# Performance work log

Hardware: AMD Instinct MI355X
Metric: run time of the kernel (lower is better)

Reference implementation:

```python
import jax, jax.numpy as jnp
import numpy as np
from jax import lax

B, CH_G, H, W = 4, 64, 240, 320
C_FEA = 8           # must equal NUM for the 'cos' branch broadcast to work (as in the original)
NUM = 8             # k_f*k_f - 1
K_G = 3
IDX_REF = NUM // 2  # 4
AFF_GAMMA = 0.5     # aff_scale_const = gamma * num = 4.0 (TGASS)


def setup_inputs() -> dict:
    key = jax.random.key(0)
    k1, k2, k3, k4, k5 = jax.random.split(key, 5)
    guidance = jax.random.normal(k1, (B, CH_G, H, W), jnp.float32)
    gt_depth_conf = jax.random.uniform(k2, (B, 1, H, W), jnp.float32)
    tgtimg_fea = jax.random.normal(k3, (B, C_FEA, H // 2, W // 2), jnp.float32)
    # torch zero-inits these; use small random weights so offsets are nontrivial
    conv_w = jax.random.normal(k4, (3 * NUM, CH_G, K_G, K_G), jnp.float32) * 0.05
    conv_b = jax.random.normal(k5, (3 * NUM,), jnp.float32) * 0.01
    aff_scale_const = jnp.full((1,), AFF_GAMMA * NUM, jnp.float32)
    return {"guidance": guidance, "gt_depth_conf": gt_depth_conf, "tgtimg_fea": tgtimg_fea,
            "conv_w": conv_w, "conv_b": conv_b, "aff_scale_const": aff_scale_const}


def _bilinear_zeros(img, x, y):
    """img: (C,Hh,Ww); x,y: (P,) absolute pixel coords. Bilinear, zero outside (== grid_sample
    align_corners=True padding_mode='zeros' and the deformable-conv im2col sampling)."""
    C, Hh, Ww = img.shape
    x0 = jnp.floor(x)
    y0 = jnp.floor(y)
    wx = x - x0
    wy = y - y0

    def g(xi, yi):
        valid = (xi >= 0) & (xi <= Ww - 1) & (yi >= 0) & (yi <= Hh - 1)
        xc = jnp.clip(xi, 0, Ww - 1).astype(jnp.int32)
        yc = jnp.clip(yi, 0, Hh - 1).astype(jnp.int32)
        return img[:, yc, xc] * valid[None].astype(img.dtype)  # (C,P)

    return (g(x0, y0) * ((1 - wy) * (1 - wx))[None]
            + g(x0 + 1, y0) * ((1 - wy) * wx)[None]
            + g(x0, y0 + 1) * (wy * (1 - wx))[None]
            + g(x0 + 1, y0 + 1) * (wy * wx)[None])


def _forward(guidance, gt_depth_conf, tgtimg_fea, conv_w, conv_b, aff_scale_const):
    Bq, _, Hh, Ww = guidance.shape
    pad = (K_G - 1) // 2
    oa = lax.conv_general_dilated(guidance, conv_w, (1, 1), [(pad, pad), (pad, pad)])
    oa = oa + conv_b[None, :, None, None]
    o1, o2, aff = jnp.split(oa, 3, axis=1)                                  # each (B,NUM,H,W)
    offset = jnp.concatenate([o1, o2], axis=1).reshape(Bq, NUM, 2, Hh, Ww)  # faithful cat+view

    # ---- cosine affinity via grid-sampling the (detached) upsampled target features ----
    fea_up = lax.stop_gradient(jax.image.resize(tgtimg_fea, (Bq, C_FEA, Hh, Ww), "bilinear"))
    xg, yg = jnp.meshgrid(jnp.arange(Hh, dtype=jnp.float32),
                          jnp.arange(Ww, dtype=jnp.float32), indexing="ij")
    # repeat_interleave along last dim: [x]*NUM then [y]*NUM
    xy = jnp.repeat(jnp.stack([xg, yg], axis=-1), NUM, axis=-1)             # (H,W,2*NUM)
    off_perm = offset.reshape(Bq, 2 * NUM, Hh, Ww).transpose(0, 2, 3, 1)    # (B,H,W,2*NUM)
    xy_off = (off_perm + xy[None]).reshape(Bq, Hh, Ww, NUM, 2)
    # original normalizes [...,0] by (W-1) and [...,1] by (H-1); with align_corners=True
    # grid_sample exactly undoes it, so [...,0] is the x/width coord, [...,1] the y/height coord
    px = xy_off[..., 0].reshape(Bq, -1)
    py = xy_off[..., 1].reshape(Bq, -1)
    sampled = jax.vmap(_bilinear_zeros)(fea_up, px, py)                     # (B,C,H*W*NUM)
    # faithful to the original's raw reshape of the (B,C,H,W*NUM) grid_sample output
    offset_feas = sampled.reshape(Bq, Hh, Ww, NUM, C_FEA).transpose(0, 3, 1, 2, 4)  # (B,NUM,H,W,C)
    fea_rep = fea_up[..., None]                                             # (B,C,H,W,1) -> bcast NUM
    cos_w = (offset_feas * fea_rep).sum(axis=1).transpose(0, 3, 1, 2)       # (B,NUM,H,W); needs C==NUM
    aff = aff * cos_w                                                       # use_aff=True

    # insert zero reference offset at center index
    zref = jnp.zeros((Bq, 1, 2, Hh, Ww), offset.dtype)
    offset_full = jnp.concatenate([offset[:, :IDX_REF], zref, offset[:, IDX_REF:]],
                                  axis=1).reshape(Bq, -1, Hh, Ww)           # (B,2*(NUM+1),H,W)

    # TGASS scaling
    aff = jnp.tanh(aff) / (aff_scale_const + 1e-8)

    # ---- confidence propagation: 1x1 modulated deform conv with w=1, b=0, modulation=1
    # == bilinear sample of gt_depth_conf at (p + offset); offsets detached in the original ----
    off_det = lax.stop_gradient(offset)
    ii = jnp.arange(Hh, dtype=jnp.float32)[:, None]
    jj = jnp.arange(Ww, dtype=jnp.float32)[None, :]
    py2 = (off_det[:, :, 0] + ii).reshape(Bq, -1)   # channel 0 = dy
    px2 = (off_det[:, :, 1] + jj).reshape(Bq, -1)   # channel 1 = dx
    conf = jax.vmap(_bilinear_zeros)(gt_depth_conf, px2, py2).reshape(Bq, NUM, Hh, Ww)
    aff = aff * conf

    # ---- normalize and build reference affinity ----
    aff_abs_sum = jnp.abs(aff).sum(axis=1, keepdims=True) + 1e-4
    aff_abs_sum = jnp.maximum(aff_abs_sum, 1.0)     # TGASS clamp
    aff = aff / aff_abs_sum
    aff_ref = 1.0 - aff.sum(axis=1, keepdims=True)
    aff_full = jnp.concatenate([aff[:, :IDX_REF], aff_ref, aff[:, IDX_REF:]], axis=1)
    aff_full = jax.nn.softmax(aff_full, axis=1)     # (B,NUM+1,H,W)
    return offset_full, aff_full


def reference(guidance, gt_depth_conf, tgtimg_fea, conv_w, conv_b, aff_scale_const):
    return _forward(guidance, gt_depth_conf, tgtimg_fea, conv_w, conv_b, aff_scale_const)
```

## Files before the change

kernel.cpp:

```cpp
#include <hip/hip_runtime.h>
#include <hip/hip_bf16.h>

typedef __hip_bfloat16 bf16;
typedef __bf16 bf16x8 __attribute__((ext_vector_type(8)));
typedef float f32x4 __attribute__((ext_vector_type(4)));

#define BB 4
#define HH 240
#define WW 320
#define CG 64
#define NCO 24
#define HWSZ (HH*WW)

__device__ __forceinline__ float ldF(const void* __restrict__ p, long i, int isbf) {
    if (isbf) return __bfloat162float(((const bf16*)p)[i]);
    return ((const float*)p)[i];
}

__device__ __forceinline__ int detect_bf16(const void* asc) {
    return ((const unsigned short*)asc)[0] != 0;
}

__device__ __forceinline__ unsigned short f2bfbits(float v) {
    bf16 h = __float2bfloat16(v);
    return *(unsigned short*)&h;
}

__device__ __forceinline__ void ld4bf(const void* __restrict__ p, long i, int isbf,
                                      unsigned short* __restrict__ o) {
    if (isbf) {
        ushort4 v = *(const ushort4*)((const unsigned short*)p + i);
        o[0] = v.x; o[1] = v.y; o[2] = v.z; o[3] = v.w;
    } else {
        float4 v = *(const float4*)((const float*)p + i);
        o[0] = f2bfbits(v.x); o[1] = f2bfbits(v.y);
        o[2] = f2bfbits(v.z); o[3] = f2bfbits(v.w);
    }
}

__global__ __launch_bounds__(256) void upsample_kernel(const void* __restrict__ tin,
                                                       const void* __restrict__ asc,
                                                       float* __restrict__ fea) {
    int isbf = detect_bf16(asc);
    int idx = blockIdx.x * 256 + threadIdx.x;
    if (idx >= BB * 8 * HWSZ) return;
    int j = idx % WW;
    int rest = idx / WW;
    int i = rest % HH;
    int bc = rest / HH;
    float sy = 0.5f * (float)i - 0.25f;
    float sx = 0.5f * (float)j - 0.25f;
    float y0f = floorf(sy), x0f = floorf(sx);
    float wy = sy - y0f, wx = sx - x0f;
    int y0 = (int)y0f, x0 = (int)x0f;
    int y0c = min(max(y0, 0), 119), y1c = min(max(y0 + 1, 0), 119);
    int x0c = min(max(x0, 0), 159), x1c = min(max(x0 + 1, 0), 159);
    long base = (long)bc * 120 * 160;
    float v00 = ldF(tin, base + y0c * 160 + x0c, isbf);
    float v01 = ldF(tin, base + y0c * 160 + x1c, isbf);
    float v10 = ldF(tin, base + y1c * 160 + x0c, isbf);
    float v11 = ldF(tin, base + y1c * 160 + x1c, isbf);
    fea[idx] = (1.f - wy) * ((1.f - wx) * v00 + wx * v01)
             + wy * ((1.f - wx) * v10 + wx * v11);
}

__global__ __launch_bounds__(256) void tgt_cl_kernel(const void* __restrict__ tin,
                                                     const void* __restrict__ asc,
                                                     float* __restrict__ tcl) {
    int isbf = detect_bf16(asc);
    int idx = blockIdx.x * 256 + threadIdx.x;
    if (idx >= BB * 8 * 120 * 160) return;
    int x = idx % 160;
    int r = idx / 160;
    int yy = r % 120;
    int rc = r / 120;
    int ch = rc % 8;
    int b = rc / 8;
    float v = ldF(tin, idx, isbf);
    tcl[((((size_t)b * 120 + yy) * 160 + x) << 3) + ch] = v;
}

__global__ __launch_bounds__(256) void upsample_cl2_kernel(const float* __restrict__ tcl,
                                                           float* __restrict__ fea_cl) {
    int idx = blockIdx.x * 256 + threadIdx.x;
    if (idx >= BB * HWSZ) return;
    int j = idx % WW;
    int rest = idx / WW;
    int i = rest % HH;
    int b = rest / HH;
    float sy = 0.5f * (float)i - 0.25f;
    float sx = 0.5f * (float)j - 0.25f;
    float y0f = floorf(sy), x0f = floorf(sx);
    float wy = sy - y0f, wx = sx - x0f;
    int y0 = (int)y0f, x0 = (int)x0f;
    int y0c = min(max(y0, 0), 119), y1c = min(max(y0 + 1, 0), 119);
    int x0c = min(max(x0, 0), 159), x1c = min(max(x0 + 1, 0), 159);

    const float* s = tcl + ((size_t)b * 120 * 160) * 8;
    const float* p00 = s + ((size_t)y0c * 160 + x0c) * 8;
    const float* p01 = s + ((size_t)y0c * 160 + x1c) * 8;
    const float* p10 = s + ((size_t)y1c * 160 + x0c) * 8;
    const float* p11 = s + ((size_t)y1c * 160 + x1c) * 8;
    float v00[8], v01[8], v10[8], v11[8], o[8];
    *(float4*)&v00[0] = *(const float4*)p00; *(float4*)&v00[4] = *(const float4*)(p00 + 4);
    *(float4*)&v01[0] = *(const float4*)p01; *(float4*)&v01[4] = *(const float4*)(p01 + 4);
    *(float4*)&v10[0] = *(const float4*)p10; *(float4*)&v10[4] = *(const float4*)(p10 + 4);
    *(float4*)&v11[0] = *(const float4*)p11; *(float4*)&v11[4] = *(const float4*)(p11 + 4);
#pragma unroll
    for (int ch = 0; ch < 8; ch++)
        o[ch] = (1.f - wy) * ((1.f - wx) * v00[ch] + wx * v01[ch])
              + wy * ((1.f - wx) * v10[ch] + wx * v11[ch]);
    float* dst = fea_cl + (size_t)idx * 8;
    *(float4*)dst = make_float4(o[0], o[1], o[2], o[3]);
    *(float4*)(dst + 4) = make_float4(o[4], o[5], o[6], o[7]);
}

__global__ __launch_bounds__(256) void prep_guidance2(const void* __restrict__ g,
                                                      const void* __restrict__ asc,
                                                      unsigned short* __restrict__ gTu) {
    int isbf = detect_bf16(asc);
    const int x0 = blockIdx.x * 64;
    const int y  = blockIdx.y;
    const int b  = blockIdx.z;
    __shared__ unsigned int sh2[64][33];
    const int t = threadIdx.x;

#pragma unroll
    for (int it = 0; it < 2; it++) {
        int cp = it * 16 + (t >> 4);
        int xq = t & 15;
        long base0 = ((long)(b * CG + 2 * cp) * HH + y) * WW + x0 + 4 * xq;
        long base1 = base0 + (long)HH * WW;
        unsigned short lo[4], hi[4];
        ld4bf(g, base0, isbf, lo);
        ld4bf(g, base1, isbf, hi);
#pragma unroll
        for (int k = 0; k < 4; k++)
            sh2[4 * xq + k][cp] = (unsigned int)lo[k] | ((unsigned int)hi[k] << 16);
    }
    __syncthreads();

#pragma unroll
    for (int it = 0; it < 2; it++) {
        int s = it * 256 + t;
        int xg = s >> 3;
        int cb = s & 7;
        int4 v = make_int4((int)sh2[xg][cb * 4 + 0], (int)sh2[xg][cb * 4 + 1],
                           (int)sh2[xg][cb * 4 + 2], (int)sh2[xg][cb * 4 + 3]);
        *(int4*)&gTu[((((long)b * HH + y) * WW + x0 + xg) << 6) + cb * 8] = v;
    }
}

__global__ __launch_bounds__(256) void prep_weights(const void* __restrict__ w,
                                                    const void* __restrict__ asc,
                                                    unsigned short* __restrict__ Bpu) {
    int isbf = detect_bf16(asc);
    int idx = blockIdx.x * 256 + threadIdx.x;
    if (idx >= 18 * 32 * 32) return;
    int t = idx >> 10;
    int r = idx & 1023;
    int n = r >> 5;
    int k = r & 31;
    int tap = t >> 1;
    int ch = t & 1;
    float v = 0.f;
    if (n < NCO)
        v = ldF(w, ((long)n * CG + ch * 32 + k) * 9 + tap, isbf);
    Bpu[idx] = f2bfbits(v);
}

__global__ __launch_bounds__(256, 4) void conv_mfma3_kernel(const unsigned short* __restrict__ gTu,
                                                            const unsigned short* __restrict__ Bpu,
                                                            const void* __restrict__ bias,
                                                            const void* __restrict__ asc,
                                                            float* __restrict__ oa,
                                                            float* __restrict__ out) {
    int isbf = detect_bf16(asc);
    const int x0 = blockIdx.x * 64;
    const int y0 = blockIdx.y * 4;
    const int b  = blockIdx.z;
    const int tid = threadIdx.x;

    __shared__ unsigned short shA[6 * 66 * 64];

#pragma unroll
    for (int it = 0; it < 13; it++) {
        int s = it * 256 + tid;
        if (s < 3168) {
            int row = s / 528;
            int rem = s - row * 528;
            int xi = rem >> 3;
            int blk = rem & 7;
            int y = y0 - 1 + row;
            int x = x0 - 1 + xi;
            int4 v = make_int4(0, 0, 0, 0);
            if (y >= 0 && y < HH && x >= 0 && x < WW)
                v = *(const int4*)(gTu + ((((size_t)b * HH + y) * WW + x) << 6)
                                       + ((blk ^ (xi & 7)) << 3));
            *(int4*)&shA[((row * 66 + xi) << 6) + (blk << 3)] = v;
        }
    }
    __syncthreads();

    const int wid  = tid >> 6;
    const int lane = tid & 63;
    const int m = lane & 15, quad = lane >> 4;

    f32x4 acc0[4], acc1[4];
#pragma unroll
    for (int r = 0; r < 4; r++) {
        acc0[r] = (f32x4){0.f, 0.f, 0.f, 0.f};
        acc1[r] = (f32x4){0.f, 0.f, 0.f, 0.f};
    }

#pragma unroll
    for (int tap = 0; tap < 9; tap++) {
        const int dy = tap / 3, dx = tap % 3;
        const int xi = wid * 16 + m + dx;
#pragma unroll
        for (int h = 0; h < 2; h++) {
            const int t = tap * 2 + h;
            int4 b0i = *(const int4*)(Bpu + ((t * 32 + m) * 32 + quad * 8));
            int4 b1i = *(const int4*)(Bpu + ((t * 32 + 16 + m) * 32 + quad * 8));
            bf16x8 bf0 = __builtin_bit_cast(bf16x8, b0i);
            bf16x8 bf1 = __builtin_bit_cast(bf16x8, b1i);
            const int sw = (((h * 4 + quad) ^ (xi & 7)) << 3);
#pragma unroll
            for (int r = 0; r < 4; r++) {
                int row = r + dy;
                int4 ai = *(const int4*)&shA[(((row * 66 + xi) << 6)) + sw];
                bf16x8 af = __builtin_bit_cast(bf16x8, ai);
                acc0[r] = __builtin_amdgcn_mfma_f32_16x16x32_bf16(af, bf0, acc0[r], 0, 0, 0);
                acc1[r] = __builtin_amdgcn_mfma_f32_16x16x32_bf16(af, bf1, acc1[r], 0, 0, 0);
            }
        }
    }

    const int n = m;
    const int x0w = x0 + wid * 16;
    float bias0 = ldF(bias, n, isbf);
    float bias1 = (n < 8) ? ldF(bias, 16 + n, isbf) : 0.f;

    __syncthreads();
    float* shO = (float*)shA;
#pragma unroll
    for (int r = 0; r < 4; r++) {
        int yy = y0 + r;
#pragma unroll
        for (int rr = 0; rr < 4; rr++) {
            int px = x0w + quad * 4 + rr;
            float v0 = acc0[r][rr] + bias0;
            float* dst = &oa[(((size_t)b * HH + yy) * WW + px) * NCO];
            dst[n] = v0;
            shO[(r * 16 + n) * 67 + (px - x0)] = v0;
            if (n < 8) dst[16 + n] = acc1[r][rr] + bias1;
        }
    }
    __syncthreads();

#pragma unroll
    for (int it = 0; it < 16; it++) {
        int s = it * 256 + tid;
        int px = s & 63;
        int rest = s >> 6;
        int nn = rest & 15;
        int r = rest >> 4;
        int och = (nn < 8) ? nn : nn + 2;
        out[(((size_t)b * 18 + och) * HH + (y0 + r)) * WW + x0 + px]
            = shO[(r * 16 + nn) * 67 + px];
    }
}

__global__ __launch_bounds__(256, 4) void conv_fallback(const void* __restrict__ g,
                                                        const void* __restrict__ w,
                                                        const void* __restrict__ bias,
                                                        const void* __restrict__ asc,
                                                        float* __restrict__ oa) {
    int isbf = detect_bf16(asc);
    const int b = blockIdx.z;
    const int i0 = blockIdx.y * 16;
    const int j0 = blockIdx.x * 16;
    const int tx = threadIdx.x & 15;
    const int ty = threadIdx.x >> 4;

    __shared__ float gl[8][18][20];
    __shared__ float wl[8][NCO][10];

    float acc[NCO];
#pragma unroll
    for (int c = 0; c < NCO; c++) acc[c] = ldF(bias, c, isbf);

    for (int ci0 = 0; ci0 < CG; ci0 += 8) {
        __syncthreads();
        for (int idx = threadIdx.x; idx < 8 * NCO * 9; idx += 256) {
            int t = idx % 9;
            int rest = idx / 9;
            int cc = rest & 7;
            int co = rest >> 3;
            wl[cc][co][t] = ldF(w, (long)(co * CG + ci0 + cc) * 9 + t, isbf);
        }
        for (int idx = threadIdx.x; idx < 8 * 18 * 18; idx += 256) {
            int cc = idx / 324;
            int rem = idx - cc * 324;
            int r = rem / 18;
            int c2 = rem - r * 18;
            int gi = i0 - 1 + r;
            int gj = j0 - 1 + c2;
            float v = 0.f;
            if (gi >= 0 && gi < HH && gj >= 0 && gj < WW)
                v = ldF(g, ((long)(b * CG + ci0 + cc) * HH + gi) * WW + gj, isbf);
            gl[cc][r][c2] = v;
        }
        __syncthreads();
#pragma unroll
        for (int cc = 0; cc < 8; cc++) {
            float ga[9];
#pragma unroll
            for (int dy = 0; dy < 3; dy++)
#pragma unroll
                for (int dx = 0; dx < 3; dx++)
                    ga[dy * 3 + dx] = gl[cc][ty + dy][tx + dx];
#pragma unroll 4
            for (int co = 0; co < NCO; co++) {
                float s = 0.f;
#pragma unroll
                for (int t = 0; t < 9; t++)
                    s += wl[cc][co][t] * ga[t];
                acc[co] += s;
            }
        }
    }
    int i = i0 + ty, j = j0 + tx;
    float4* p = (float4*)&oa[(((size_t)b * HH + i) * WW + j) * NCO];
#pragma unroll
    for (int q = 0; q < 6; q++)
        p[q] = make_float4(acc[4 * q], acc[4 * q + 1], acc[4 * q + 2], acc[4 * q + 3]);
}

__device__ __forceinline__ float bil_zero_f32(const float* __restrict__ img,
                                              float x, float y) {
    float x0f = floorf(x), y0f = floorf(y);
    float wx = x - x0f, wy = y - y0f;
    int x0 = (int)x0f, y0 = (int)y0f;
    int x0c = min(max(x0, 0), WW - 1), x1c = min(max(x0 + 1, 0), WW - 1);
    int y0c = min(max(y0, 0), HH - 1), y1c = min(max(y0 + 1, 0), HH - 1);
    float mx0 = (x0 == x0c) ? 1.f : 0.f;
    float mx1 = (x0 + 1 == x1c) ? 1.f : 0.f;
    float my0 = (y0 == y0c) ? 1.f : 0.f;
    float my1 = (y0 + 1 == y1c) ? 1.f : 0.f;
    const float* r0 = img + (size_t)y0c * WW;
    const float* r1 = img + (size_t)y1c * WW;
    float v00 = r0[x0c], v01 = r0[x1c], v10 = r1[x0c], v11 = r1[x1c];
    return my0 * (1.f - wy) * (mx0 * (1.f - wx) * v00 + mx1 * wx * v01)
         + my1 * wy * (mx0 * (1.f - wx) * v10 + mx1 * wx * v11);
}

__device__ __forceinline__ float bil_zero_poly(const void* __restrict__ img, long base,
                                               float x, float y, int isbf) {
    float x0f = floorf(x), y0f = floorf(y);
    float wx = x - x0f, wy = y - y0f;
    int x0 = (int)x0f, y0 = (int)y0f;
    int x0c = min(max(x0, 0), WW - 1), x1c = min(max(x0 + 1, 0), WW - 1);
    int y0c = min(max(y0, 0), HH - 1), y1c = min(max(y0 + 1, 0), HH - 1);
    float mx0 = (x0 == x0c) ? 1.f : 0.f;
    float mx1 = (x0 + 1 == x1c) ? 1.f : 0.f;
    float my0 = (y0 == y0c) ? 1.f : 0.f;
    float my1 = (y0 + 1 == y1c) ? 1.f : 0.f;
    long r0 = base + (long)y0c * WW;
    long r1 = base + (long)y1c * WW;
    float v00 = ldF(img, r0 + x0c, isbf), v01 = ldF(img, r0 + x1c, isbf);
    float v10 = ldF(img, r1 + x0c, isbf), v11 = ldF(img, r1 + x1c, isbf);
    return my0 * (1.f - wy) * (mx0 * (1.f - wx) * v00 + mx1 * wx * v01)
         + my1 * wy * (mx0 * (1.f - wx) * v10 + mx1 * wx * v11);
}

__global__ __launch_bounds__(256, 4) void cos_kernel(const float* __restrict__ oa,
                                                     const float* __restrict__ fea_cl,
                                                     float* __restrict__ cos_buf) {
    __shared__ float S_lds[64 * 65];
    const int bx = blockIdx.x;
    const int pi = blockIdx.y;
    const int b  = blockIdx.z;
    const int tid = threadIdx.x;
    const int qj_l = tid & 63;
    const int cpair = tid >> 6;
    const int qj = bx * 64 + qj_l;

    const float* feaB = fea_cl + (size_t)b * HWSZ * 8;
    const float4 ov = *(const float4*)&oa[(((size_t)b * HH + pi) * WW + qj) * NCO + 4 * cpair];

#pragma unroll
    for (int t = 0; t < 2; t++) {
        int c = 2 * cpair + t;
        float ox = (t == 0) ? ov.x : ov.z;
        float oy = (t == 0) ? ov.y : ov.w;
        float add = (c < 4) ? (float)pi : (float)qj;
        float px = ox + add, py = oy + add;

        float x0f = floorf(px), y0f = floorf(py);
        float wx = px - x0f, wy = py - y0f;
        int x0 = (int)x0f, y0 = (int)y0f;
        int x0c = min(max(x0, 0), WW - 1), x1c = min(max(x0 + 1, 0), WW - 1);
        int y0c = min(max(y0, 0), HH - 1), y1c = min(max(y0 + 1, 0), HH - 1);
        float mx0 = (x0 == x0c) ? 1.f : 0.f;
        float mx1 = (x0 + 1 == x1c) ? 1.f : 0.f;
        float my0 = (y0 == y0c) ? 1.f : 0.f;
        float my1 = (y0 + 1 == y1c) ? 1.f : 0.f;
        float aw = mx0 * (1.f - wx);
        float bw = mx1 * wx;
        float tw = my0 * (1.f - wy);
        float dw = my1 * wy;

        const float* r0 = feaB + (size_t)y0c * WW * 8;
        const float* r1 = feaB + (size_t)y1c * WW * 8;
        float v00[8], v01[8], v10[8], v11[8];
        *(float4*)&v00[0] = *(const float4*)(r0 + x0c * 8);
        *(float4*)&v00[4] = *(const float4*)(r0 + x0c * 8 + 4);
        *(float4*)&v01[0] = *(const float4*)(r0 + x1c * 8);
        *(float4*)&v01[4] = *(const float4*)(r0 + x1c * 8 + 4);
        *(float4*)&v10[0] = *(const float4*)(r1 + x0c * 8);
        *(float4*)&v10[4] = *(const float4*)(r1 + x0c * 8 + 4);
        *(float4*)&v11[0] = *(const float4*)(r1 + x1c * 8);
        *(float4*)&v11[4] = *(const float4*)(r1 + x1c * 8 + 4);

        int base = qj_l * 65 + c * 8;
#pragma unroll
        for (int ch = 0; ch < 8; ch++)
            S_lds[base + ch] = tw * (aw * v00[ch] + bw * v01[ch])
                             + dw * (aw * v10[ch] + bw * v11[ch]);
    }

    __syncthreads();

    {
        int pix = tid >> 2;
        int cp  = tid & 3;
        int g = pix >> 3;
        int c_img = pix & 7;
        int i = c_img * 30 + (pi >> 3);
        int j = (pi & 7) * 40 + bx * 8 + g;
        const float* fp = feaB + ((size_t)i * WW + j) * 8;
        float f[8];
        *(float4*)&f[0] = *(const float4*)fp;
        *(float4*)&f[4] = *(const float4*)(fp + 4);
        float a0 = 0.f, a1 = 0.f;
        int c0 = 2 * cp;
#pragma unroll
        for (int n = 0; n < 8; n++) {
            float fn = f[n];
            int rb = (8 * g + n) * 65 + c_img;
            a0 += fn * S_lds[rb + c0 * 8];
            a1 += fn * S_lds[rb + (c0 + 1) * 8];
        }
        float* dst = cos_buf + (((size_t)b * HH + i) * WW + j) * 8 + c0;
        *(float2*)dst = make_float2(a0, a1);
    }
}

__global__ __launch_bounds__(256, 4) void final3_kernel(const float* __restrict__ oa,
                                                        const float* __restrict__ cos_buf,
                                                        const void* __restrict__ conf_in,
                                                        const void* __restrict__ asc_p,
                                                        float* __restrict__ out) {
    int isbf = detect_bf16(asc_p);
    int idx = blockIdx.x * 256 + threadIdx.x;
    if (idx >= BB * HWSZ) return;
    int j = idx % WW;
    int rest = idx / WW;
    int i = rest % HH;
    int b = rest / HH;

    float cos_acc[8];
    {
        const float* cp = cos_buf + (size_t)idx * 8;
        float4 ca = *(const float4*)cp;
        float4 cb = *(const float4*)(cp + 4);
        cos_acc[0] = ca.x; cos_acc[1] = ca.y; cos_acc[2] = ca.z; cos_acc[3] = ca.w;
        cos_acc[4] = cb.x; cos_acc[5] = cb.y; cos_acc[6] = cb.z; cos_acc[7] = cb.w;
    }

    const float4* op = (const float4*)&oa[(((size_t)b * HH + i) * WW + j) * NCO];
    float own[24];
#pragma unroll
    for (int q = 0; q < 6; q++) {
        float4 v = op[q];
        own[4 * q] = v.x; own[4 * q + 1] = v.y; own[4 * q + 2] = v.z; own[4 * q + 3] = v.w;
    }

    float asc = ldF(asc_p, 0, isbf) + 1e-8f;
    long cbase = (long)b * HWSZ;

    float a[8];
    float ssum = 0.f;
#pragma unroll
    for (int c = 0; c < 8; c++) {
        float v = own[16 + c] * cos_acc[c];
        v = tanhf(v) / asc;
        float py2 = own[2 * c] + (float)i;
        float px2 = own[2 * c + 1] + (float)j;
        float cf = bil_zero_poly(conf_in, cbase, px2, py2, isbf);
        v *= cf;
        a[c] = v;
        ssum += fabsf(v);
    }
    ssum += 1e-4f;
    ssum = fmaxf(ssum, 1.0f);
    float inv = 1.0f / ssum;
    float asum = 0.f;
#pragma unroll
    for (int c = 0; c < 8; c++) { a[c] *= inv; asum += a[c]; }
    float aref = 1.0f - asum;

    float vals[9];
#pragma unroll
    for (int c = 0; c < 4; c++) vals[c] = a[c];
    vals[4] = aref;
#pragma unroll
    for (int c = 4; c < 8; c++) vals[c + 1] = a[c];
    float m = vals[0];
#pragma unroll
    for (int k = 1; k < 9; k++) m = fmaxf(m, vals[k]);
    float es = 0.f;
#pragma unroll
    for (int k = 0; k < 9; k++) { vals[k] = __expf(vals[k] - m); es += vals[k]; }
    float ei = 1.0f / es;

    size_t pix = (size_t)i * WW + j;
    size_t base_o = (size_t)b * 18 * HWSZ + pix;
    out[base_o + (size_t)8 * HWSZ] = 0.f;
    out[base_o + (size_t)9 * HWSZ] = 0.f;
    float* aff_out = out + (size_t)BB * 18 * HWSZ;
    size_t base_a = (size_t)b * 9 * HWSZ + pix;
#pragma unroll
    for (int k = 0; k < 9; k++)
        aff_out[base_a + (size_t)k * HWSZ] = vals[k] * ei;
}

__global__ __launch_bounds__(256, 4) void final2_kernel(const float* __restrict__ oa,
                                                        const float* __restrict__ cos_buf,
                                                        const void* __restrict__ conf_in,
                                                        const void* __restrict__ asc_p,
                                                        float* __restrict__ out) {
    int isbf = detect_bf16(asc_p);
    int idx = blockIdx.x * 256 + threadIdx.x;
    if (idx >= BB * HWSZ) return;
    int j = idx % WW;
    int rest = idx / WW;
    int i = rest % HH;
    int b = rest / HH;

    float cos_acc[8];
    {
        const float* cp = cos_buf + (size_t)idx * 8;
        float4 ca = *(const float4*)cp;
        float4 cb = *(const float4*)(cp + 4);
        cos_acc[0] = ca.x; cos_acc[1] = ca.y; cos_acc[2] = ca.z; cos_acc[3] = ca.w;
        cos_acc[4] = cb.x; cos_acc[5] = cb.y; cos_acc[6] = cb.z; cos_acc[7] = cb.w;
    }

    const float4* op = (const float4*)&oa[(((size_t)b * HH + i) * WW + j) * NCO];
    float own[24];
#pragma unroll
    for (int q = 0; q < 6; q++) {
        float4 v = op[q];
        own[4 * q] = v.x; own[4 * q + 1] = v.y; own[4 * q + 2] = v.z; own[4 * q + 3] = v.w;
    }

    float asc = ldF(asc_p, 0, isbf) + 1e-8f;
    long cbase = (long)b * HWSZ;

    float a[8];
    float ssum = 0.f;
#pragma unroll
    for (int c = 0; c < 8; c++) {
        float v = own[16 + c] * cos_acc[c];
        v = tanhf(v) / asc;
        float py2 = own[2 * c] + (float)i;
        float px2 = own[2 * c + 1] + (float)j;
        float cf = bil_zero_poly(conf_in, cbase, px2, py2, isbf);
        v *= cf;
        a[c] = v;
        ssum += fabsf(v);
    }
    ssum += 1e-4f;
    ssum = fmaxf(ssum, 1.0f);
    float inv = 1.0f / ssum;
    float asum = 0.f;
#pragma unroll
    for (int c = 0; c < 8; c++) { a[c] *= inv; asum += a[c]; }
    float aref = 1.0f - asum;

    float vals[9];
#pragma unroll
    for (int c = 0; c < 4; c++) vals[c] = a[c];
    vals[4] = aref;
#pragma unroll
    for (int c = 4; c < 8; c++) vals[c + 1] = a[c];
    float m = vals[0];
#pragma unroll
    for (int k = 1; k < 9; k++) m = fmaxf(m, vals[k]);
    float es = 0.f;
#pragma unroll
    for (int k = 0; k < 9; k++) { vals[k] = __expf(vals[k] - m); es += vals[k]; }
    float ei = 1.0f / es;

    size_t pix = (size_t)i * WW + j;
    size_t base_o = (size_t)b * 18 * HWSZ + pix;
#pragma unroll
    for (int ch = 0; ch < 18; ch++) {
        float v;
        if (ch < 8) v = own[ch];
        else if (ch < 10) v = 0.f;
        else v = own[ch - 2];
        out[base_o + (size_t)ch * HWSZ] = v;
    }
    float* aff_out = out + (size_t)BB * 18 * HWSZ;
    size_t base_a = (size_t)b * 9 * HWSZ + pix;
#pragma unroll
    for (int k = 0; k < 9; k++)
        aff_out[base_a + (size_t)k * HWSZ] = vals[k] * ei;
}

__global__ __launch_bounds__(256, 4) void final_kernel(const float* __restrict__ oa,
                                                       const float* __restrict__ fea,
                                                       const void* __restrict__ conf_in,
                                                       const void* __restrict__ asc_p,
                                                       float* __restrict__ out) {
    int isbf = detect_bf16(asc_p);
    int idx = blockIdx.x * 256 + threadIdx.x;
    if (idx >= BB * HWSZ) return;
    int j = idx % WW;
    int rest = idx / WW;
    int i = rest % HH;
    int b = rest / HH;

    const float* feaB = fea + (size_t)b * 8 * HWSZ;
    float f[8];
#pragma unroll
    for (int n = 0; n < 8; n++)
        f[n] = feaB[(size_t)n * HWSZ + (size_t)i * WW + j];

    int c_img = i / 30;
    int pi = (i % 30) * 8 + j / 40;
    int pj0 = (j % 40) * 8;
    const float* feaC = feaB + (size_t)c_img * HWSZ;

    float cos_acc[8];
#pragma unroll
    for (int c = 0; c < 8; c++) cos_acc[c] = 0.f;

#pragma unroll 1
    for (int n = 0; n < 8; n++) {
        int qj = pj0 + n;
        const float4* oq = (const float4*)&oa[(((size_t)b * HH + pi) * WW + qj) * NCO];
        float4 o0 = oq[0], o1 = oq[1], o2 = oq[2], o3 = oq[3];
        float off[16] = {o0.x, o0.y, o0.z, o0.w, o1.x, o1.y, o1.z, o1.w,
                         o2.x, o2.y, o2.z, o2.w, o3.x, o3.y, o3.z, o3.w};
        float fn = f[n];
#pragma unroll
        for (int c = 0; c < 8; c++) {
            float add = (c < 4) ? (float)pi : (float)qj;
            float px = off[2 * c] + add;
            float py = off[2 * c + 1] + add;
            cos_acc[c] += fn * bil_zero_f32(feaC, px, py);
        }
    }

    const float4* op = (const float4*)&oa[(((size_t)b * HH + i) * WW + j) * NCO];
    float own[24];
#pragma unroll
    for (int q = 0; q < 6; q++) {
        float4 v = op[q];
        own[4 * q] = v.x; own[4 * q + 1] = v.y; own[4 * q + 2] = v.z; own[4 * q + 3] = v.w;
    }

    float asc = ldF(asc_p, 0, isbf) + 1e-8f;
    long cbase = (long)b * HWSZ;

    float a[8];
    float ssum = 0.f;
#pragma unroll
    for (int c = 0; c < 8; c++) {
        float v = own[16 + c] * cos_acc[c];
        v = tanhf(v) / asc;
        float py2 = own[2 * c] + (float)i;
        float px2 = own[2 * c + 1] + (float)j;
        float cf = bil_zero_poly(conf_in, cbase, px2, py2, isbf);
        v *= cf;
        a[c] = v;
        ssum += fabsf(v);
    }
    ssum += 1e-4f;
    ssum = fmaxf(ssum, 1.0f);
    float inv = 1.0f / ssum;
    float asum = 0.f;
#pragma unroll
    for (int c = 0; c < 8; c++) { a[c] *= inv; asum += a[c]; }
    float aref = 1.0f - asum;

    float vals[9];
#pragma unroll
    for (int c = 0; c < 4; c++) vals[c] = a[c];
    vals[4] = aref;
#pragma unroll
    for (int c = 4; c < 8; c++) vals[c + 1] = a[c];
    float m = vals[0];
#pragma unroll
    for (int k = 1; k < 9; k++) m = fmaxf(m, vals[k]);
    float es = 0.f;
#pragma unroll
    for (int k = 0; k < 9; k++) { vals[k] = __expf(vals[k] - m); es += vals[k]; }
    float ei = 1.0f / es;

    size_t pix = (size_t)i * WW + j;
    size_t base_o = (size_t)b * 18 * HWSZ + pix;
#pragma unroll
    for (int ch = 0; ch < 18; ch++) {
        float v;
        if (ch < 8) v = own[ch];
        else if (ch < 10) v = 0.f;
        else v = own[ch - 2];
        out[base_o + (size_t)ch * HWSZ] = v;
    }
    float* aff_out = out + (size_t)BB * 18 * HWSZ;
    size_t base_a = (size_t)b * 9 * HWSZ + pix;
#pragma unroll
    for (int k = 0; k < 9; k++)
        aff_out[base_a + (size_t)k * HWSZ] = vals[k] * ei;
}

extern "C" void kernel_launch(void* const* d_in, const int* in_sizes, int n_in,
                              void* d_out, int out_size, void* d_ws, size_t ws_size,
                              hipStream_t stream) {
    const void* guidance = d_in[0];
    const void* gtconf   = d_in[1];
    const void* tgt      = d_in[2];
    const void* conv_w   = d_in[3];
    const void* conv_b   = d_in[4];
    const void* asc      = d_in[5];

    float* oa  = (float*)d_ws;
    float* fea = oa + (size_t)BB * HWSZ * NCO;
    float* big = fea + (size_t)BB * 8 * HWSZ;
    unsigned short* gTu = (unsigned short*)big;
    float* cosb = big;
    float* tcl  = big;
    unsigned short* Bpu = (unsigned short*)((char*)big + (size_t)39321600);
    const size_t ws_full = (size_t)29491200 + 9830400 + 39321600 + 36864;
    const size_t ws_mid  = (size_t)29491200 + 9830400 + 9830400;
    float* out = (float*)d_out;

    int n_pix = BB * HWSZ;
    int n_tgt = BB * 8 * 120 * 160;

    if (ws_size >= ws_full) {
        tgt_cl_kernel<<<(n_tgt + 255) / 256, 256, 0, stream>>>(tgt, asc, tcl);
        upsample_cl2_kernel<<<(n_pix + 255) / 256, 256, 0, stream>>>(tcl, fea);
        prep_weights<<<72, 256, 0, stream>>>(conv_w, asc, Bpu);
        dim3 pgrid(WW / 64, HH, BB);
        prep_guidance2<<<pgrid, 256, 0, stream>>>(guidance, asc, gTu);
        dim3 cgrid(WW / 64, HH / 4, BB);
        conv_mfma3_kernel<<<cgrid, 256, 0, stream>>>(gTu, Bpu, conv_b, asc, oa, out);
        dim3 ggrid(WW / 64, HH, BB);
        cos_kernel<<<ggrid, 256, 0, stream>>>(oa, fea, cosb);
        final3_kernel<<<(n_pix + 255) / 256, 256, 0, stream>>>(oa, cosb, gtconf, asc, out);
    } else if (ws_size >= ws_mid) {
        tgt_cl_kernel<<<(n_tgt + 255) / 256, 256, 0, stream>>>(tgt, asc, tcl);
        upsample_cl2_kernel<<<(n_pix + 255) / 256, 256, 0, stream>>>(tcl, fea);
        dim3 cgrid(WW / 16, HH / 16, BB);
        conv_fallback<<<cgrid, 256, 0, stream>>>(guidance, conv_w, conv_b, asc, oa);
        dim3 ggrid(WW / 64, HH, BB);
        cos_kernel<<<ggrid, 256, 0, stream>>>(oa, fea, cosb);
        final2_kernel<<<(n_pix + 255) / 256, 256, 0, stream>>>(oa, cosb, gtconf, asc, out);
    } else {
        int n_up = BB * 8 * HWSZ;
        upsample_kernel<<<(n_up + 255) / 256, 256, 0, stream>>>(tgt, asc, fea);
        dim3 cgrid(WW / 16, HH / 16, BB);
        conv_fallback<<<cgrid, 256, 0, stream>>>(guidance, conv_w, conv_b, asc, oa);
        final_kernel<<<(n_pix + 255) / 256, 256, 0, stream>>>(oa, fea, gtconf, asc, out);
    }
}
```

Before: 236.3 us.

## Fuse cosine-similarity sampling into the MFMA conv kernel epilogue

```diff
diff --git a/kernel.cpp b/kernel.cpp
--- a/kernel.cpp
+++ b/kernel.cpp
@@ -169,19 +169,24 @@
     Bpu[idx] = f2bfbits(v);
 }
 
-__global__ __launch_bounds__(256, 4) void conv_mfma3_kernel(const unsigned short* __restrict__ gTu,
+__global__ __launch_bounds__(256, 4) void conv_mfma4_kernel(const unsigned short* __restrict__ gTu,
                                                             const unsigned short* __restrict__ Bpu,
                                                             const void* __restrict__ bias,
                                                             const void* __restrict__ asc,
+                                                            const float* __restrict__ fea_cl,
                                                             float* __restrict__ oa,
+                                                            float* __restrict__ cosb,
                                                             float* __restrict__ out) {
     int isbf = detect_bf16(asc);
     const int x0 = blockIdx.x * 64;
     const int y0 = blockIdx.y * 4;
     const int b  = blockIdx.z;
     const int tid = threadIdx.x;
+    const int bx = blockIdx.x;
 
     __shared__ unsigned short shA[6 * 66 * 64];
+    float* shO = (float*)shA;
+    float* S   = (float*)((char*)shA + 17408);
 
 #pragma unroll
     for (int it = 0; it < 13; it++) {
@@ -242,7 +247,6 @@
     float bias1 = (n < 8) ? ldF(bias, 16 + n, isbf) : 0.f;
 
     __syncthreads();
-    float* shO = (float*)shA;
 #pragma unroll
     for (int r = 0; r < 4; r++) {
         int yy = y0 + r;
@@ -268,6 +272,81 @@
         int och = (nn < 8) ? nn : nn + 2;
         out[(((size_t)b * 18 + och) * HH + (y0 + r)) * WW + x0 + px]
             = shO[(r * 16 + nn) * 67 + px];
+    }
+
+    const float* feaB = fea_cl + (size_t)b * HWSZ * 8;
+#pragma unroll 1
+    for (int r = 0; r < 4; r++) {
+        const int pi = y0 + r;
+#pragma unroll
+        for (int k = 0; k < 2; k++) {
+            int s = k * 256 + tid;
+            int c = s >> 6;
+            int qj_l = s & 63;
+            int qj = x0 + qj_l;
+            float ox = shO[(r * 16 + 2 * c) * 67 + qj_l];
+            float oy = shO[(r * 16 + 2 * c + 1) * 67 + qj_l];
+            float add = (c < 4) ? (float)pi : (float)qj;
+            float px = ox + add, py = oy + add;
+
+            float x0f = floorf(px), y0f = floorf(py);
+            float wx = px - x0f, wy = py - y0f;
+            int xx0 = (int)x0f, yy0 = (int)y0f;
+            int x0c = min(max(xx0, 0), WW - 1), x1c = min(max(xx0 + 1, 0), WW - 1);
+            int y0c = min(max(yy0, 0), HH - 1), y1c = min(max(yy0 + 1, 0), HH - 1);
+            float mx0 = (xx0 == x0c) ? 1.f : 0.f;
+            float mx1 = (xx0 + 1 == x1c) ? 1.f : 0.f;
+            float my0 = (yy0 == y0c) ? 1.f : 0.f;
+            float my1 = (yy0 + 1 == y1c) ? 1.f : 0.f;
+            float aw = mx0 * (1.f - wx);
+            float bw = mx1 * wx;
+            float tw = my0 * (1.f - wy);
+            float dw = my1 * wy;
+
+            const float* r0 = feaB + (size_t)y0c * WW * 8;
+            const float* r1 = feaB + (size_t)y1c * WW * 8;
+            float v00[8], v01[8], v10[8], v11[8];
+            *(float4*)&v00[0] = *(const float4*)(r0 + x0c * 8);
+            *(float4*)&v00[4] = *(const float4*)(r0 + x0c * 8 + 4);
+            *(float4*)&v01[0] = *(const float4*)(r0 + x1c * 8);
+            *(float4*)&v01[4] = *(const float4*)(r0 + x1c * 8 + 4);
+            *(float4*)&v10[0] = *(const float4*)(r1 + x0c * 8);
+            *(float4*)&v10[4] = *(const float4*)(r1 + x0c * 8 + 4);
+            *(float4*)&v11[0] = *(const float4*)(r1 + x1c * 8);
+            *(float4*)&v11[4] = *(const float4*)(r1 + x1c * 8 + 4);
+
+            int base = qj_l * 65 + c * 8;
+#pragma unroll
+            for (int ch = 0; ch < 8; ch++)
+                S[base + ch] = tw * (aw * v00[ch] + bw * v01[ch])
+                             + dw * (aw * v10[ch] + bw * v11[ch]);
+        }
+        __syncthreads();
+
+        {
+            int pix = tid >> 2;
+            int cp  = tid & 3;
+            int g = pix >> 3;
+            int c_img = pix & 7;
+            int i = c_img * 30 + (pi >> 3);
+            int j = (pi & 7) * 40 + bx * 8 + g;
+            const float* fp = feaB + ((size_t)i * WW + j) * 8;
+            float f[8];
+            *(float4*)&f[0] = *(const float4*)fp;
+            *(float4*)&f[4] = *(const float4*)(fp + 4);
+            float a0 = 0.f, a1 = 0.f;
+            int c0 = 2 * cp;
+#pragma unroll
+            for (int nn = 0; nn < 8; nn++) {
+                float fn = f[nn];
+                int rb = (8 * g + nn) * 65 + c_img;
+                a0 += fn * S[rb + c0 * 8];
+                a1 += fn * S[rb + (c0 + 1) * 8];
+            }
+            float* dst = cosb + (((size_t)b * HH + i) * WW + j) * 8 + c0;
+            *(float2*)dst = make_float2(a0, a1);
+        }
+        __syncthreads();
     }
 }
 
@@ -495,7 +574,8 @@
 #pragma unroll
     for (int c = 0; c < 8; c++) {
         float v = own[16 + c] * cos_acc[c];
-        v = tanhf(v) / asc;
+        float e2 = __expf(2.f * v);
+        v = (1.f - 2.f / (e2 + 1.f)) / asc;
         float py2 = own[2 * c] + (float)i;
         float px2 = own[2 * c + 1] + (float)j;
         float cf = bil_zero_poly(conf_in, cbase, px2, py2, isbf);
@@ -739,14 +819,14 @@
     const void* conv_b   = d_in[4];
     const void* asc      = d_in[5];
 
-    float* oa  = (float*)d_ws;
-    float* fea = oa + (size_t)BB * HWSZ * NCO;
-    float* big = fea + (size_t)BB * 8 * HWSZ;
+    float* oa   = (float*)d_ws;
+    float* fea  = oa + (size_t)BB * HWSZ * NCO;
+    float* cosb = fea + (size_t)BB * 8 * HWSZ;
+    float* big  = cosb + (size_t)BB * 8 * HWSZ;
     unsigned short* gTu = (unsigned short*)big;
-    float* cosb = big;
     float* tcl  = big;
     unsigned short* Bpu = (unsigned short*)((char*)big + (size_t)39321600);
-    const size_t ws_full = (size_t)29491200 + 9830400 + 39321600 + 36864;
+    const size_t ws_full = (size_t)29491200 + 9830400 + 9830400 + 39321600 + 36864;
     const size_t ws_mid  = (size_t)29491200 + 9830400 + 9830400;
     float* out = (float*)d_out;
 
@@ -760,13 +840,12 @@
         dim3 pgrid(WW / 64, HH, BB);
         prep_guidance2<<<pgrid, 256, 0, stream>>>(guidance, asc, gTu);
         dim3 cgrid(WW / 64, HH / 4, BB);
-        conv_mfma3_kernel<<<cgrid, 256, 0, stream>>>(gTu, Bpu, conv_b, asc, oa, out);
-        dim3 ggrid(WW / 64, HH, BB);
-        cos_kernel<<<ggrid, 256, 0, stream>>>(oa, fea, cosb);
+        conv_mfma4_kernel<<<cgrid, 256, 0, stream>>>(gTu, Bpu, conv_b, asc, fea, oa, cosb, out);
         final3_kernel<<<(n_pix + 255) / 256, 256, 0, stream>>>(oa, cosb, gtconf, asc, out);
     } else if (ws_size >= ws_mid) {
-        tgt_cl_kernel<<<(n_tgt + 255) / 256, 256, 0, stream>>>(tgt, asc, tcl);
-        upsample_cl2_kernel<<<(n_pix + 255) / 256, 256, 0, stream>>>(tcl, fea);
+        float* tclm = cosb;
+        tgt_cl_kernel<<<(n_tgt + 255) / 256, 256, 0, stream>>>(tgt, asc, tclm);
+        upsample_cl2_kernel<<<(n_pix + 255) / 256, 256, 0, stream>>>(tclm, fea);
         dim3 cgrid(WW / 16, HH / 16, BB);
         conv_fallback<<<cgrid, 256, 0, stream>>>(guidance, conv_w, conv_b, asc, oa);
         dim3 ggrid(WW / 64, HH, BB);
```

Result: faster. 218.4 us (-7.6%).
